# Kernel tuning notes

Hardware: AMD Instinct MI355X
Metric: run time of the kernel (lower is better)

Reference implementation:

```python
import jax, jax.numpy as jnp
import numpy as np

# HT config: input_shape = output_shape = (8,8,8,8), rank = 8, d = 4 modes
B = 4096
M = 8      # per-mode input dim
N = 8      # per-mode output dim
R = 8      # HT rank
FEAT = M ** 4  # 4096


def setup_inputs() -> dict:
    key = jax.random.key(0)
    ks = jax.random.split(key, 8)
    x = jax.random.normal(ks[0], (B, FEAT), dtype=jnp.float32)
    # leaf factors: (in_p, out_p, rank); xavier-style scale over the input mode
    f_std = np.float32(np.sqrt(2.0 / (M + N * R)))
    F0 = jax.random.normal(ks[1], (M, N, R), dtype=jnp.float32) * f_std
    F1 = jax.random.normal(ks[2], (M, N, R), dtype=jnp.float32) * f_std
    F2 = jax.random.normal(ks[3], (M, N, R), dtype=jnp.float32) * f_std
    F3 = jax.random.normal(ks[4], (M, N, R), dtype=jnp.float32) * f_std
    # internal cores: (left_rank, right_rank, parent_rank)
    c_std = np.float32(np.sqrt(2.0 / (R + R * R)))
    CL = jax.random.normal(ks[5], (R, R, R), dtype=jnp.float32) * c_std
    CR = jax.random.normal(ks[6], (R, R, R), dtype=jnp.float32) * c_std
    bound = np.float32(1.0 / np.sqrt(FEAT))
    bias = jax.random.uniform(ks[7], (FEAT,), dtype=jnp.float32, minval=-bound, maxval=bound)
    return {"x": x, "F0": F0, "F1": F1, "F2": F2, "F3": F3,
            "CL": CL, "CR": CR, "bias": bias}


def reference(x, F0, F1, F2, F3, CL, CR, bias):
    b = x.shape[0]
    # (b, i, j, k, l): one axis per HT mode
    x4 = x.reshape(b, M, M, M, M)
    # Pre-contract each subtree's two leaves with its core (tiny tensors):
    # left transfer  W_L[i, j, a, c, p], right transfer W_R[k, l, d, e, p].
    # This is the same tensor-network contraction as the tn.Node graph,
    # just in an efficient associativity order.
    WL = jnp.einsum('iar,jcs,rsp->ijacp', F0, F1, CL)
    WR = jnp.einsum('kdr,les,rsp->kldep', F2, F3, CR)
    # contract left subtree against the input: (b, k, l, a, c, p)
    yL = jnp.einsum('bijkl,ijacp->bklacp', x4, WL)
    # contract right subtree; parent edges of the two subtrees are joined (p)
    y = jnp.einsum('bklacp,kldep->bacde', yL, WR)
    return y.reshape(b, FEAT) + bias
```

## Files before the change

### kernel.cpp

```cpp
#include <hip/hip_runtime.h>
#include <hip/hip_bf16.h>


typedef short bf16x8 __attribute__((ext_vector_type(8)));
typedef float f32x16 __attribute__((ext_vector_type(16)));

union Frag8 {
    bf16x8 v;
    unsigned int u4[4];
};

static __device__ __forceinline__ unsigned int pkbf(float a, float b) {
    __hip_bfloat162 h = __float22bfloat162_rn(float2{a, b});
    return *reinterpret_cast<unsigned int*>(&h);
}

__global__ __launch_bounds__(256) void ht_precompute(
        const float* __restrict__ F0, const float* __restrict__ F1,
        const float* __restrict__ F2, const float* __restrict__ F3,
        const float* __restrict__ CL, const float* __restrict__ CR,
        unsigned short* __restrict__ frags) {
    __shared__ float sFa[512], sFb[512], sC[512], sG[512];
    const int isW = blockIdx.x >> 3;
    const int p   = blockIdx.x & 7;
    const float* Fa = isW ? F2 : F0;
    const float* Fb = isW ? F3 : F1;
    const float* C  = isW ? CR : CL;
    const int tid = threadIdx.x;

    for (int u = tid; u < 512; u += 256) {
        sFa[u] = Fa[u]; sFb[u] = Fb[u]; sC[u] = C[u];
    }
    __syncthreads();

#pragma unroll
    for (int e = 0; e < 2; ++e) {
        int u = tid + e * 256;
        int r = u >> 6, jc = u & 63;
        float acc = 0.f;
#pragma unroll
        for (int s = 0; s < 8; ++s)
            acc += sFb[jc * 8 + s] * sC[(r * 8 + s) * 8 + p];
        sG[u] = acc;
    }
    __syncthreads();

#pragma unroll
    for (int e = 0; e < 2; ++e) {
        int g  = tid + e * 256;
        int i1 = g >> 6, n = g & 63;
        int a  = n >> 3, c = n & 7;
        float fa[8];
#pragma unroll
        for (int r = 0; r < 8; ++r) fa[r] = sFa[(i1 * 8 + a) * 8 + r];
        unsigned int pk[4];
#pragma unroll
        for (int jp = 0; jp < 4; ++jp) {
            float o0 = 0.f, o1 = 0.f;
#pragma unroll
            for (int r = 0; r < 8; ++r) {
                o0 += fa[r] * sG[r * 64 + (2 * jp) * 8 + c];
                o1 += fa[r] * sG[r * 64 + (2 * jp + 1) * 8 + c];
            }
            pk[jp] = pkbf(o0, o1);
        }
        int t = n >> 5, kc = i1 >> 1, lane_ = (i1 & 1) * 32 + (n & 31);
        unsigned int* dst = (unsigned int*)(frags + (size_t)isW * 32768 +
                                            ((((p * 2 + t) * 4 + kc) << 6) + lane_) * 8);
        *(uint4*)dst = uint4{pk[0], pk[1], pk[2], pk[3]};
    }
}

#define Y_PITCH 66

__global__ __launch_bounds__(256, 2) void ht_main(const float* __restrict__ x,
                                                  const unsigned short* __restrict__ frags,
                                                  const float* __restrict__ bias,
                                                  float* __restrict__ out) {
    __shared__ __align__(16) char smem[34816];
    const int tid  = threadIdx.x;
    const int lane = tid & 63;
    const int w    = __builtin_amdgcn_readfirstlane(tid >> 6);
    const int b    = blockIdx.x * 4 + w;
    const int l31  = lane & 31;
    const int hi   = lane >> 5;

    Frag8 xf[2][4];
    const float* xb = x + ((size_t)b << 12);
#pragma unroll
    for (int rb = 0; rb < 2; ++rb)
#pragma unroll
        for (int kc = 0; kc < 4; ++kc) {
            const float* src = xb + (kc * 16 + hi * 8) * 64 + rb * 32 + l31;
#pragma unroll
            for (int j = 0; j < 8; j += 2)
                xf[rb][kc].u4[j >> 1] = pkbf(src[j * 64], src[(j + 1) * 64]);
        }

    f32x16 acc[2][2];
#pragma unroll
    for (int i = 0; i < 2; ++i)
#pragma unroll
        for (int j = 0; j < 2; ++j)
#pragma unroll
            for (int e = 0; e < 16; ++e)
                acc[i][j][e] = 0.f;

    auto stage_issue = [&](int buf, int pn) {
        const char* gA = (const char*)frags + pn * 8192 + w * 2048 + lane * 16;
        const char* gW = (const char*)frags + 65536 + pn * 8192 + w * 2048 + lane * 16;
        char* lA = smem + buf * 16384 + w * 2048;
        char* lW = smem + buf * 16384 + 8192 + w * 2048;
        __builtin_amdgcn_global_load_lds((const __attribute__((address_space(1))) void*)gA,
                                         (__attribute__((address_space(3))) void*)lA, 16, 0, 0);
        __builtin_amdgcn_global_load_lds((const __attribute__((address_space(1))) void*)(gA + 1024),
                                         (__attribute__((address_space(3))) void*)(lA + 1024), 16, 0, 0);
        __builtin_amdgcn_global_load_lds((const __attribute__((address_space(1))) void*)gW,
                                         (__attribute__((address_space(3))) void*)lW, 16, 0, 0);
        __builtin_amdgcn_global_load_lds((const __attribute__((address_space(1))) void*)(gW + 1024),
                                         (__attribute__((address_space(3))) void*)(lW + 1024), 16, 0, 0);
    };

    stage_issue(0, 0);

#pragma unroll
    for (int p = 0; p < 8; ++p) {
        if (p < 7) {
            stage_issue((p + 1) & 1, p + 1);
            asm volatile("s_waitcnt vmcnt(4)" ::: "memory");
        } else {
            asm volatile("s_waitcnt vmcnt(0)" ::: "memory");
        }
        __builtin_amdgcn_s_barrier();

        const unsigned short* LB = (const unsigned short*)(smem + (p & 1) * 16384);
        Frag8 af[2][4], wf[2][4];
#pragma unroll
        for (int t = 0; t < 2; ++t)
#pragma unroll
            for (int kc = 0; kc < 4; ++kc) {
                af[t][kc].v = *(const bf16x8*)(LB + (t * 4 + kc) * 512 + lane * 8);
                wf[t][kc].v = *(const bf16x8*)(LB + 4096 + (t * 4 + kc) * 512 + lane * 8);
            }
#pragma unroll
        for (int rb = 0; rb < 2; ++rb) {
#pragma unroll
            for (int cb = 0; cb < 2; ++cb) {
                f32x16 t;
#pragma unroll
                for (int e = 0; e < 16; ++e) t[e] = 0.f;
#pragma unroll
                for (int kc = 0; kc < 4; ++kc)
                    t = __builtin_amdgcn_mfma_f32_32x32x16_bf16(xf[rb][kc].v, af[cb][kc].v, t, 0, 0, 0);
                unsigned int wd[8];
#pragma unroll
                for (int h = 0; h < 8; ++h) wd[h] = pkbf(t[2 * h], t[2 * h + 1]);
                auto s02 = __builtin_amdgcn_permlane32_swap(wd[0], wd[2], false, false);
                auto s13 = __builtin_amdgcn_permlane32_swap(wd[1], wd[3], false, false);
                auto s46 = __builtin_amdgcn_permlane32_swap(wd[4], wd[6], false, false);
                auto s57 = __builtin_amdgcn_permlane32_swap(wd[5], wd[7], false, false);
                Frag8 tb0, tb1;
                tb0.u4[0] = s02[0]; tb0.u4[1] = s13[0]; tb0.u4[2] = s02[1]; tb0.u4[3] = s13[1];
                tb1.u4[0] = s46[0]; tb1.u4[1] = s57[0]; tb1.u4[2] = s46[1]; tb1.u4[3] = s57[1];
                acc[0][cb] = __builtin_amdgcn_mfma_f32_32x32x16_bf16(wf[0][2 * rb].v,     tb0.v, acc[0][cb], 0, 0, 0);
                acc[0][cb] = __builtin_amdgcn_mfma_f32_32x32x16_bf16(wf[0][2 * rb + 1].v, tb1.v, acc[0][cb], 0, 0, 0);
                acc[1][cb] = __builtin_amdgcn_mfma_f32_32x32x16_bf16(wf[1][2 * rb].v,     tb0.v, acc[1][cb], 0, 0, 0);
                acc[1][cb] = __builtin_amdgcn_mfma_f32_32x32x16_bf16(wf[1][2 * rb + 1].v, tb1.v, acc[1][cb], 0, 0, 0);
            }
        }
        __builtin_amdgcn_s_barrier();
    }

    float* Yw = (float*)smem + w * (32 * Y_PITCH);
    float* ob = out + ((size_t)b << 12);
#pragma unroll
    for (int cb = 0; cb < 2; ++cb) {
#pragma unroll
        for (int mt = 0; mt < 2; ++mt)
#pragma unroll
            for (int rp = 0; rp < 8; ++rp) {
                int de = mt * 32 + 8 * (rp >> 1) + 2 * (rp & 1) + 4 * hi;
                float2 v;
                v.x = acc[mt][cb][2 * rp];
                v.y = acc[mt][cb][2 * rp + 1];
                *(float2*)(&Yw[l31 * Y_PITCH + de]) = v;
            }
#pragma unroll
        for (int i = 0; i < 16; ++i) {
            int acl = 2 * i + hi;
            float2 v = *(float2*)(&Yw[acl * Y_PITCH + 2 * l31]);
            int o = (cb * 32 + acl) * 64 + 2 * l31;
            float2 bv = *(const float2*)(bias + o);
            v.x += bv.x;
            v.y += bv.y;
            *(float2*)(ob + o) = v;
        }
    }
}

extern "C" void kernel_launch(void* const* d_in, const int* in_sizes, int n_in,
                              void* d_out, int out_size, void* d_ws, size_t ws_size,
                              hipStream_t stream) {
    const float* x    = (const float*)d_in[0];
    const float* F0   = (const float*)d_in[1];
    const float* F1   = (const float*)d_in[2];
    const float* F2   = (const float*)d_in[3];
    const float* F3   = (const float*)d_in[4];
    const float* CL   = (const float*)d_in[5];
    const float* CR   = (const float*)d_in[6];
    const float* bias = (const float*)d_in[7];
    float* out = (float*)d_out;
    unsigned short* frags = (unsigned short*)d_ws;

    const int B = in_sizes[0] / 4096;

    ht_precompute<<<16, 256, 0, stream>>>(F0, F1, F2, F3, CL, CR, frags);
    ht_main<<<B / 4, 256, 0, stream>>>(x, frags, bias, out);
}
```

Measured before the change: 147.6 us.

## Stage all HT fragments and bias in LDS once; loop batches per wave

Each 512-thread block now loads the full set of precomputed transfer fragments and the bias into LDS once. Each wave then processes two batch rows with a register prefetch of the next row's x, which replaces the per-step double-buffered fragment streaming and its barriers. The second MFMA's operand order is swapped so accumulators map straight to output rows, removing the LDS transpose in the epilogue. In exchange, the 144KB LDS footprint limits residency to one block per CU, and the x prefetch adds register pressure.

After: 210.4 us. 42.6% more time.

```diff
diff --git a/kernel.cpp b/kernel.cpp
--- a/kernel.cpp
+++ b/kernel.cpp
@@ -71,130 +71,132 @@
     }
 }
 
-#define Y_PITCH 66
-
-__global__ __launch_bounds__(256, 2) void ht_main(const float* __restrict__ x,
+#define NB 2
+
+__global__ __launch_bounds__(512, 2) void ht_main(const float* __restrict__ x,
                                                   const unsigned short* __restrict__ frags,
                                                   const float* __restrict__ bias,
                                                   float* __restrict__ out) {
-    __shared__ __align__(16) char smem[34816];
+    __shared__ __align__(16) char smem[147456];
     const int tid  = threadIdx.x;
     const int lane = tid & 63;
     const int w    = __builtin_amdgcn_readfirstlane(tid >> 6);
-    const int b    = blockIdx.x * 4 + w;
     const int l31  = lane & 31;
     const int hi   = lane >> 5;
-
-    Frag8 xf[2][4];
-    const float* xb = x + ((size_t)b << 12);
-#pragma unroll
-    for (int rb = 0; rb < 2; ++rb)
-#pragma unroll
-        for (int kc = 0; kc < 4; ++kc) {
-            const float* src = xb + (kc * 16 + hi * 8) * 64 + rb * 32 + l31;
-#pragma unroll
-            for (int j = 0; j < 8; j += 2)
-                xf[rb][kc].u4[j >> 1] = pkbf(src[j * 64], src[(j + 1) * 64]);
+    const int b0   = blockIdx.x * (8 * NB) + w * NB;
+
+    float xr[64];
+    {
+        const float* xb = x + ((size_t)b0 << 12);
+#pragma unroll
+        for (int rb = 0; rb < 2; ++rb)
+#pragma unroll
+            for (int kc = 0; kc < 4; ++kc)
+#pragma unroll
+                for (int j = 0; j < 8; ++j)
+                    xr[(rb * 4 + kc) * 8 + j] = xb[(kc * 16 + hi * 8 + j) * 64 + rb * 32 + l31];
+    }
+#pragma unroll
+    for (int r = 0; r < 16; ++r)
+        __builtin_amdgcn_global_load_lds(
+            (const __attribute__((address_space(1))) void*)((const char*)frags + r * 8192 + tid * 16),
+            (__attribute__((address_space(3))) void*)(smem + r * 8192 + tid * 16), 16, 0, 0);
+#pragma unroll
+    for (int r = 0; r < 2; ++r)
+        __builtin_amdgcn_global_load_lds(
+            (const __attribute__((address_space(1))) void*)((const char*)bias + r * 8192 + tid * 16),
+            (__attribute__((address_space(3))) void*)(smem + 131072 + r * 8192 + tid * 16), 16, 0, 0);
+    __syncthreads();
+
+    const unsigned short* LA = (const unsigned short*)smem;
+    const unsigned short* LW = (const unsigned short*)(smem + 65536);
+    const float* sBias = (const float*)(smem + 131072);
+
+#pragma unroll 1
+    for (int i = 0; i < NB; ++i) {
+        const int b = b0 + i;
+        Frag8 xf[2][4];
+#pragma unroll
+        for (int rb = 0; rb < 2; ++rb)
+#pragma unroll
+            for (int kc = 0; kc < 4; ++kc)
+#pragma unroll
+                for (int jp = 0; jp < 4; ++jp)
+                    xf[rb][kc].u4[jp] = pkbf(xr[(rb * 4 + kc) * 8 + 2 * jp],
+                                             xr[(rb * 4 + kc) * 8 + 2 * jp + 1]);
+        if (i + 1 < NB) {
+            const float* xb = x + ((size_t)(b + 1) << 12);
+#pragma unroll
+            for (int rb = 0; rb < 2; ++rb)
+#pragma unroll
+                for (int kc = 0; kc < 4; ++kc)
+#pragma unroll
+                    for (int j = 0; j < 8; ++j)
+                        xr[(rb * 4 + kc) * 8 + j] = xb[(kc * 16 + hi * 8 + j) * 64 + rb * 32 + l31];
         }
 
-    f32x16 acc[2][2];
-#pragma unroll
-    for (int i = 0; i < 2; ++i)
-#pragma unroll
-        for (int j = 0; j < 2; ++j)
-#pragma unroll
-            for (int e = 0; e < 16; ++e)
-                acc[i][j][e] = 0.f;
-
-    auto stage_issue = [&](int buf, int pn) {
-        const char* gA = (const char*)frags + pn * 8192 + w * 2048 + lane * 16;
-        const char* gW = (const char*)frags + 65536 + pn * 8192 + w * 2048 + lane * 16;
-        char* lA = smem + buf * 16384 + w * 2048;
-        char* lW = smem + buf * 16384 + 8192 + w * 2048;
-        __builtin_amdgcn_global_load_lds((const __attribute__((address_space(1))) void*)gA,
-                                         (__attribute__((address_space(3))) void*)lA, 16, 0, 0);
-        __builtin_amdgcn_global_load_lds((const __attribute__((address_space(1))) void*)(gA + 1024),
-                                         (__attribute__((address_space(3))) void*)(lA + 1024), 16, 0, 0);
-        __builtin_amdgcn_global_load_lds((const __attribute__((address_space(1))) void*)gW,
-                                         (__attribute__((address_space(3))) void*)lW, 16, 0, 0);
-        __builtin_amdgcn_global_load_lds((const __attribute__((address_space(1))) void*)(gW + 1024),
-                                         (__attribute__((address_space(3))) void*)(lW + 1024), 16, 0, 0);
-    };
-
-    stage_issue(0, 0);
-
-#pragma unroll
-    for (int p = 0; p < 8; ++p) {
-        if (p < 7) {
-            stage_issue((p + 1) & 1, p + 1);
-            asm volatile("s_waitcnt vmcnt(4)" ::: "memory");
-        } else {
-            asm volatile("s_waitcnt vmcnt(0)" ::: "memory");
-        }
-        __builtin_amdgcn_s_barrier();
-
-        const unsigned short* LB = (const unsigned short*)(smem + (p & 1) * 16384);
-        Frag8 af[2][4], wf[2][4];
-#pragma unroll
-        for (int t = 0; t < 2; ++t)
-#pragma unroll
-            for (int kc = 0; kc < 4; ++kc) {
-                af[t][kc].v = *(const bf16x8*)(LB + (t * 4 + kc) * 512 + lane * 8);
-                wf[t][kc].v = *(const bf16x8*)(LB + 4096 + (t * 4 + kc) * 512 + lane * 8);
-            }
-#pragma unroll
-        for (int rb = 0; rb < 2; ++rb) {
-#pragma unroll
-            for (int cb = 0; cb < 2; ++cb) {
-                f32x16 t;
-#pragma unroll
-                for (int e = 0; e < 16; ++e) t[e] = 0.f;
+        f32x16 acc[2][2];
+#pragma unroll
+        for (int a = 0; a < 2; ++a)
+#pragma unroll
+            for (int c = 0; c < 2; ++c)
+#pragma unroll
+                for (int e = 0; e < 16; ++e)
+                    acc[a][c][e] = 0.f;
+
+#pragma unroll 2
+        for (int p = 0; p < 8; ++p) {
+            Frag8 af[2][4];
+#pragma unroll
+            for (int t = 0; t < 2; ++t)
 #pragma unroll
                 for (int kc = 0; kc < 4; ++kc)
-                    t = __builtin_amdgcn_mfma_f32_32x32x16_bf16(xf[rb][kc].v, af[cb][kc].v, t, 0, 0, 0);
-                unsigned int wd[8];
-#pragma unroll
-                for (int h = 0; h < 8; ++h) wd[h] = pkbf(t[2 * h], t[2 * h + 1]);
-                auto s02 = __builtin_amdgcn_permlane32_swap(wd[0], wd[2], false, false);
-                auto s13 = __builtin_amdgcn_permlane32_swap(wd[1], wd[3], false, false);
-                auto s46 = __builtin_amdgcn_permlane32_swap(wd[4], wd[6], false, false);
-                auto s57 = __builtin_amdgcn_permlane32_swap(wd[5], wd[7], false, false);
-                Frag8 tb0, tb1;
-                tb0.u4[0] = s02[0]; tb0.u4[1] = s13[0]; tb0.u4[2] = s02[1]; tb0.u4[3] = s13[1];
-                tb1.u4[0] = s46[0]; tb1.u4[1] = s57[0]; tb1.u4[2] = s46[1]; tb1.u4[3] = s57[1];
-                acc[0][cb] = __builtin_amdgcn_mfma_f32_32x32x16_bf16(wf[0][2 * rb].v,     tb0.v, acc[0][cb], 0, 0, 0);
-                acc[0][cb] = __builtin_amdgcn_mfma_f32_32x32x16_bf16(wf[0][2 * rb + 1].v, tb1.v, acc[0][cb], 0, 0, 0);
-                acc[1][cb] = __builtin_amdgcn_mfma_f32_32x32x16_bf16(wf[1][2 * rb].v,     tb0.v, acc[1][cb], 0, 0, 0);
-                acc[1][cb] = __builtin_amdgcn_mfma_f32_32x32x16_bf16(wf[1][2 * rb + 1].v, tb1.v, acc[1][cb], 0, 0, 0);
+                    af[t][kc].v = *(const bf16x8*)(LA + p * 4096 + ((t * 4 + kc) * 64 + lane) * 8);
+#pragma unroll
+            for (int rb = 0; rb < 2; ++rb) {
+                Frag8 wfr[2][2];
+#pragma unroll
+                for (int t = 0; t < 2; ++t)
+#pragma unroll
+                    for (int kk = 0; kk < 2; ++kk)
+                        wfr[t][kk].v = *(const bf16x8*)(LW + p * 4096 + ((t * 4 + 2 * rb + kk) * 64 + lane) * 8);
+#pragma unroll
+                for (int cb = 0; cb < 2; ++cb) {
+                    f32x16 t;
+#pragma unroll
+                    for (int e = 0; e < 16; ++e) t[e] = 0.f;
+#pragma unroll
+                    for (int kc = 0; kc < 4; ++kc)
+                        t = __builtin_amdgcn_mfma_f32_32x32x16_bf16(xf[rb][kc].v, af[cb][kc].v, t, 0, 0, 0);
+                    unsigned int wd[8];
+#pragma unroll
+                    for (int h = 0; h < 8; ++h) wd[h] = pkbf(t[2 * h], t[2 * h + 1]);
+                    auto s02 = __builtin_amdgcn_permlane32_swap(wd[0], wd[2], false, false);
+                    auto s13 = __builtin_amdgcn_permlane32_swap(wd[1], wd[3], false, false);
+                    auto s46 = __builtin_amdgcn_permlane32_swap(wd[4], wd[6], false, false);
+                    auto s57 = __builtin_amdgcn_permlane32_swap(wd[5], wd[7], false, false);
+                    Frag8 tb0, tb1;
+                    tb0.u4[0] = s02[0]; tb0.u4[1] = s13[0]; tb0.u4[2] = s02[1]; tb0.u4[3] = s13[1];
+                    tb1.u4[0] = s46[0]; tb1.u4[1] = s57[0]; tb1.u4[2] = s46[1]; tb1.u4[3] = s57[1];
+                    acc[cb][0] = __builtin_amdgcn_mfma_f32_32x32x16_bf16(tb0.v, wfr[0][0].v, acc[cb][0], 0, 0, 0);
+                    acc[cb][0] = __builtin_amdgcn_mfma_f32_32x32x16_bf16(tb1.v, wfr[0][1].v, acc[cb][0], 0, 0, 0);
+                    acc[cb][1] = __builtin_amdgcn_mfma_f32_32x32x16_bf16(tb0.v, wfr[1][0].v, acc[cb][1], 0, 0, 0);
+                    acc[cb][1] = __builtin_amdgcn_mfma_f32_32x32x16_bf16(tb1.v, wfr[1][1].v, acc[cb][1], 0, 0, 0);
+                }
             }
         }
-        __builtin_amdgcn_s_barrier();
-    }
-
-    float* Yw = (float*)smem + w * (32 * Y_PITCH);
-    float* ob = out + ((size_t)b << 12);
-#pragma unroll
-    for (int cb = 0; cb < 2; ++cb) {
-#pragma unroll
-        for (int mt = 0; mt < 2; ++mt)
-#pragma unroll
-            for (int rp = 0; rp < 8; ++rp) {
-                int de = mt * 32 + 8 * (rp >> 1) + 2 * (rp & 1) + 4 * hi;
-                float2 v;
-                v.x = acc[mt][cb][2 * rp];
-                v.y = acc[mt][cb][2 * rp + 1];
-                *(float2*)(&Yw[l31 * Y_PITCH + de]) = v;
-            }
-#pragma unroll
-        for (int i = 0; i < 16; ++i) {
-            int acl = 2 * i + hi;
-            float2 v = *(float2*)(&Yw[acl * Y_PITCH + 2 * l31]);
-            int o = (cb * 32 + acl) * 64 + 2 * l31;
-            float2 bv = *(const float2*)(bias + o);
-            v.x += bv.x;
-            v.y += bv.y;
-            *(float2*)(ob + o) = v;
-        }
+
+        float* ob = out + ((size_t)b << 12);
+#pragma unroll
+        for (int cb = 0; cb < 2; ++cb)
+#pragma unroll
+            for (int nb2 = 0; nb2 < 2; ++nb2)
+#pragma unroll
+                for (int r = 0; r < 16; ++r) {
+                    int ac = cb * 32 + (r & 3) + 8 * (r >> 2) + 4 * hi;
+                    int o  = ac * 64 + nb2 * 32 + l31;
+                    ob[o] = acc[cb][nb2][r] + sBias[o];
+                }
     }
 }
 
@@ -215,5 +217,5 @@
     const int B = in_sizes[0] / 4096;
 
     ht_precompute<<<16, 256, 0, stream>>>(F0, F1, F2, F3, CL, CR, frags);
-    ht_main<<<B / 4, 256, 0, stream>>>(x, frags, bias, out);
-}
+    ht_main<<<B / (8 * NB), 512, 0, stream>>>(x, frags, bias, out);
+}
```
